# Optimization experiments

Hardware: AMD Instinct MI355X
Metric: run time of the kernel (lower is better)

Reference implementation:

```python
import jax, jax.numpy as jnp
import numpy as np

N = 50000      # nodes
E = 800000     # edges
D_IN = 128
D_H = 512
D_OUT = 256
G = 512        # graphs in batch
EPS_GIN = 0.0  # GINConv default eps
LRELU_SLOPE = 1.5


def setup_inputs() -> dict:
    key = jax.random.key(0)
    ks = jax.random.split(key, 16)
    x = jax.random.normal(ks[0], (N, D_IN), dtype=jnp.float32)
    edge_index = jax.random.randint(ks[1], (2, E), 0, N, dtype=jnp.int64)
    batch = jnp.sort(jax.random.randint(ks[2], (N,), 0, G, dtype=jnp.int64))
    def lin(k, fan_in, fan_out):
        bound = 1.0 / np.sqrt(fan_in)
        k1, k2 = jax.random.split(k)
        W = jax.random.uniform(k1, (fan_in, fan_out), jnp.float32, -bound, bound)
        b = jax.random.uniform(k2, (fan_out,), jnp.float32, -bound, bound)
        return W, b
    W1, b1 = lin(ks[3], D_IN, D_H)
    W2, b2 = lin(ks[4], D_H, D_H)
    W3, b3 = lin(ks[5], D_H, D_H)
    W4, b4 = lin(ks[6], D_H, D_H)
    Wl, bl = lin(ks[7], D_H, D_OUT)
    return {"x": x, "edge_index": edge_index, "batch": batch,
            "W1": W1, "b1": b1, "W2": W2, "b2": b2,
            "W3": W3, "b3": b3, "W4": W4, "b4": b4,
            "Wl": Wl, "bl": bl}


def reference(x, edge_index, batch, W1, b1, W2, b2, W3, b3, W4, b4, Wl, bl):
    # GIN aggregation: sum neighbor (source) features at each target node
    src, dst = edge_index[0], edge_index[1]
    agg = jax.ops.segment_sum(x[src], dst, num_segments=N)  # [N, D_IN]
    h = (1.0 + EPS_GIN) * x + agg
    # 4-layer MLP (Dropout inactive in eval; LeakyReLU negative_slope=1.5)
    h = h @ W1 + b1
    h = jnp.where(h > 0, h, LRELU_SLOPE * h)
    h = jax.nn.relu(h @ W2 + b2)
    h = jax.nn.relu(h @ W3 + b3)
    h = h @ W4 + b4                      # [N, D_H]
    # global mean pool over graphs
    sums = jax.ops.segment_sum(h, batch, num_segments=G)          # [G, D_H]
    cnt = jax.ops.segment_sum(jnp.ones((N, 1), h.dtype), batch, num_segments=G)
    pooled = sums / jnp.maximum(cnt, 1.0)
    out = pooled @ Wl + bl               # [G, D_OUT]
    # F.normalize(dim=1, eps=1e-12)
    nrm = jnp.linalg.norm(out, axis=1, keepdims=True)
    return out / jnp.maximum(nrm, 1e-12)
```

## Files before the change

kernel.cpp:

```cpp
#include <hip/hip_runtime.h>
#include <hip/hip_bf16.h>
#include <cstdint>
#include <cstddef>

#define N_NODES 50000
#define N_EDGES 800000
#define D_IN 128
#define D_H 512
#define D_OUT 256
#define N_GRAPHS 512

#define BM 128
#define BN 256
#define BK 32
#define NBLK ((N_NODES + 255) / 256)
#define CT_SW 264
#define N_MT 391
#define MT_PER_XCD 49

#define NBUCK 196
#define BCAP 6144
#define E_PER_BLK 4096

#define XQ_SCALE 4096.0f
#define XQ_INV (1.0f / 4096.0f)

typedef __bf16 v8bf __attribute__((ext_vector_type(8)));
typedef float v4f __attribute__((ext_vector_type(4)));
typedef int v4i __attribute__((ext_vector_type(4)));

__device__ __forceinline__ float bf2f(unsigned short b) {
  return __uint_as_float(((unsigned int)b) << 16);
}
__device__ __forceinline__ unsigned short f2bf(float f) {
  unsigned int u = __float_as_uint(f);
  u += 0x7FFFu + ((u >> 16) & 1u);
  return (unsigned short)(u >> 16);
}

__device__ __forceinline__ void gload_lds16(const void* g, void* l) {
  __builtin_amdgcn_global_load_lds(
      (const __attribute__((address_space(1))) void*)g,
      (__attribute__((address_space(3))) void*)l, 16, 0, 0);
}

__global__ __launch_bounds__(256) void k_prep(const void* __restrict__ x,
                                              const void* __restrict__ ei,
                                              const void* __restrict__ batch,
                                              int* __restrict__ gcur,
                                              int* __restrict__ flags) {
  __shared__ int cnt[3];
  int t = threadIdx.x;
  gcur[t] = 0;
  if (t < 3) cnt[t] = 0;
  __syncthreads();
  const unsigned short* xs = (const unsigned short*)x;
  int c0 = 0;
  for (int k = t; k < 4096; k += 256) {
    unsigned int e = (xs[k] >> 7) & 0xFFu;
    if (e >= 0x90u) c0++;
  }
  atomicAdd(&cnt[0], c0);
  const int* e32 = (const int*)ei;
  int c1 = 0;
  for (int k = t; k < 512; k += 256)
    if (e32[2 * k + 1] != 0) c1++;
  atomicAdd(&cnt[1], c1);
  const int* b32 = (const int*)batch;
  int c2 = 0;
  {
    int w = (N_NODES - 512) + 2 * t + 1;
    if (b32[w] != 0) c2++;
  }
  atomicAdd(&cnt[2], c2);
  __syncthreads();
  if (t == 0) {
    flags[0] = (cnt[0] > 16) ? 1 : 0;
    flags[1] = (cnt[1] == 0) ? 1 : 0;
    flags[2] = (cnt[2] == 0) ? 1 : 0;
  }
}

__global__ __launch_bounds__(256) void k_transpose_all(
    const void* W1, const void* W2, const void* W3, const void* W4,
    const void* Wl, unsigned short* W1T, unsigned short* W2T,
    unsigned short* W3T, unsigned short* W4T, unsigned short* WlT,
    const int* __restrict__ flags) {
  __shared__ unsigned short tile[64][65];
  int bid = blockIdx.x;
  const void* src;
  unsigned short* dst;
  int R, C, tb;
  if (bid < 16)        { src = W1; dst = W1T; R = 128; C = 512; tb = bid; }
  else if (bid < 80)   { src = W2; dst = W2T; R = 512; C = 512; tb = bid - 16; }
  else if (bid < 144)  { src = W3; dst = W3T; R = 512; C = 512; tb = bid - 80; }
  else if (bid < 208)  { src = W4; dst = W4T; R = 512; C = 512; tb = bid - 144; }
  else                 { src = Wl; dst = WlT; R = 512; C = 256; tb = bid - 208; }
  int tpr = C >> 6;
  int r0 = (tb / tpr) << 6, c0 = (tb % tpr) << 6;
  int t = threadIdx.x;
  bool f32 = flags[0] != 0;
#pragma unroll
  for (int k = 0; k < 16; ++k) {
    int idx = k * 256 + t;
    int r = idx >> 6, c = idx & 63;
    unsigned short v =
        f32 ? f2bf(((const float*)src)[(size_t)(r0 + r) * C + c0 + c])
            : ((const unsigned short*)src)[(size_t)(r0 + r) * C + c0 + c];
    tile[c][r] = v;
  }
  __syncthreads();
#pragma unroll
  for (int k = 0; k < 16; ++k) {
    int idx = k * 256 + t;
    int r = idx >> 6, c = idx & 63;
    dst[(size_t)(c0 + r) * R + r0 + c] = tile[r][c];
  }
}

__global__ __launch_bounds__(256) void k_cvtx(const void* __restrict__ x,
                                              const int* __restrict__ flags,
                                              unsigned int* __restrict__ xi) {
  int i = blockIdx.x * 256 + threadIdx.x;
  if (i >= N_NODES * D_IN / 2) {
    if (i < N_NODES * D_IN / 2 + 64) xi[i] = 0;
    return;
  }
  float v0, v1;
  if (flags[0]) {
    const float* xf = (const float*)x + (size_t)i * 2;
    v0 = xf[0];
    v1 = xf[1];
  } else {
    unsigned int p = ((const unsigned int*)x)[i];
    v0 = __uint_as_float((p & 0xFFFFu) << 16);
    v1 = __uint_as_float(p & 0xFFFF0000u);
  }
  int q0 = __float2int_rn(fminf(fmaxf(v0, -7.99f), 7.99f) * XQ_SCALE);
  int q1 = __float2int_rn(fminf(fmaxf(v1, -7.99f), 7.99f) * XQ_SCALE);
  xi[i] = ((unsigned int)q0 & 0xFFFFu) | ((unsigned int)q1 << 16);
}

__global__ __launch_bounds__(256) void kb_scatter(
    const int* __restrict__ ei, const int* __restrict__ flags,
    int* __restrict__ gcur, unsigned int* __restrict__ pairs, int ne) {
  __shared__ int hist[256];
  __shared__ int sstart[256];
  __shared__ int gbase[256];
  __shared__ int sh[256];
  __shared__ unsigned int lbuf[E_PER_BLK];
  int t = threadIdx.x;
  int e0 = blockIdx.x * E_PER_BLK;
  int nloc = ne - e0;
  if (nloc > E_PER_BLK) nloc = E_PER_BLK;
  hist[t] = 0;
  __syncthreads();
  bool fe64 = flags[1] != 0;
  unsigned int pk[16];
  short bk[16], rk[16];
#pragma unroll
  for (int it = 0; it < 16; ++it) {
    int li = it * 256 + t;
    bk[it] = -1;
    if (li < nloc) {
      size_t e = (size_t)e0 + li;
      int s = fe64 ? ei[2 * e] : ei[e];
      int d = fe64 ? ei[2 * ((size_t)ne + e)] : ei[(size_t)ne + e];
      int b = d >> 8;
      pk[it] = (unsigned int)(s & 0xFFFF) | ((unsigned int)(d & 255) << 16) |
               ((unsigned int)b << 24);
      bk[it] = (short)b;
      rk[it] = (short)atomicAdd(&hist[b], 1);
    }
  }
  __syncthreads();
  int cnt = hist[t];
  sh[t] = cnt;
  __syncthreads();
  for (int o = 1; o < 256; o <<= 1) {
    int a = sh[t];
    int bb = (t >= o) ? sh[t - o] : 0;
    __syncthreads();
    sh[t] = a + bb;
    __syncthreads();
  }
  sstart[t] = sh[t] - cnt;
  gbase[t] = (cnt > 0) ? atomicAdd(&gcur[t], cnt) : 0;
  __syncthreads();
#pragma unroll
  for (int it = 0; it < 16; ++it)
    if (bk[it] >= 0) lbuf[sstart[bk[it]] + rk[it]] = pk[it];
  __syncthreads();
  for (int i = t; i < nloc; i += 256) {
    unsigned int v = lbuf[i];
    int b = v >> 24;
    int off = gbase[b] + (i - sstart[b]);
    if (off < BCAP) pairs[(size_t)b * BCAP + off] = v;
  }
}

__global__ __launch_bounds__(256) void kb_sort(
    const unsigned int* __restrict__ pairs, const int* __restrict__ gcur,
    int* __restrict__ rowptr, unsigned short* __restrict__ elist) {
  __shared__ int sh[256];
  __shared__ int cursor[256];
  __shared__ unsigned int lpair[BCAP];
  __shared__ unsigned short sorted[BCAP];
  int b = blockIdx.x, t = threadIdx.x;
  int c = (t < NBUCK) ? gcur[t] : 0;
  if (c > BCAP) c = BCAP;
  sh[t] = c;
  __syncthreads();
  for (int o = 1; o < 256; o <<= 1) {
    int a = sh[t];
    int v = (t >= o) ? sh[t - o] : 0;
    __syncthreads();
    sh[t] = a + v;
    __syncthreads();
  }
  int base = (b == 0) ? 0 : sh[b - 1];
  int cnt = sh[b] - base;
  cursor[t] = 0;
  __syncthreads();
  for (int i = t; i < cnt; i += 256) {
    unsigned int v = pairs[(size_t)b * BCAP + i];
    lpair[i] = v;
    atomicAdd(&cursor[(v >> 16) & 255], 1);
  }
  __syncthreads();
  int nc = cursor[t];
  sh[t] = nc;
  __syncthreads();
  for (int o = 1; o < 256; o <<= 1) {
    int a = sh[t];
    int v = (t >= o) ? sh[t - o] : 0;
    __syncthreads();
    sh[t] = a + v;
    __syncthreads();
  }
  int nstart = sh[t] - nc;
  cursor[t] = nstart;
  int node = b * 256 + t;
  if (node <= N_NODES) rowptr[node] = base + nstart;
  __syncthreads();
  for (int i = t; i < cnt; i += 256) {
    unsigned int v = lpair[i];
    int r = atomicAdd(&cursor[(v >> 16) & 255], 1);
    sorted[r] = (unsigned short)(v & 0xFFFFu);
  }
  __syncthreads();
  for (int i = t; i < cnt; i += 256)
    elist[base + i] = sorted[i];
}

__global__ __launch_bounds__(256) void k_gather(
    const unsigned int* __restrict__ xi, const int* __restrict__ rowptr,
    const unsigned short* __restrict__ elist, unsigned int* __restrict__ h0) {
  int node = blockIdx.x * 4 + (threadIdx.x >> 6);
  if (node >= N_NODES) return;
  int lane = threadIdx.x & 63;
  int l15 = lane & 15;
  int grp = lane >> 4;
  int s0 = rowptr[node], s1 = rowptr[node + 1];
  int a[8];
  {
    v4i self = (v4i){0, 0, 0, 0};
    if (lane < 16) self = *(const v4i*)(xi + (size_t)node * 64 + l15 * 4);
#pragma unroll
    for (int q = 0; q < 4; ++q) {
      a[2 * q]     = (int)(short)(self[q] & 0xFFFF);
      a[2 * q + 1] = self[q] >> 16;
    }
  }
  for (int j0 = s0; j0 < s1; j0 += 64) {
    int jj = j0 + lane;
    int cnt = s1 - j0;
    cnt = cnt < 64 ? cnt : 64;
    int ev = (jj < s1) ? (int)elist[jj] : N_NODES;
    for (int j = 0; j < cnt; j += 4) {
      int src = __shfl(ev, j + grp, 64);
      v4i p = *(const v4i*)(xi + (size_t)src * 64 + l15 * 4);
#pragma unroll
      for (int q = 0; q < 4; ++q) {
        a[2 * q]     += (int)(short)(p[q] & 0xFFFF);
        a[2 * q + 1] += p[q] >> 16;
      }
    }
  }
#pragma unroll
  for (int k = 0; k < 8; ++k) {
    a[k] += __shfl_xor(a[k], 16, 64);
    a[k] += __shfl_xor(a[k], 32, 64);
  }
  if (lane < 16) {
    v4i o;
#pragma unroll
    for (int q = 0; q < 4; ++q) {
      unsigned int lo = f2bf((float)a[2 * q] * XQ_INV);
      unsigned int hi = f2bf((float)a[2 * q + 1] * XQ_INV);
      o[q] = (int)(lo | (hi << 16));
    }
    *(v4i*)(h0 + (size_t)node * 64 + l15 * 4) = o;
  }
}

template <int ACT, bool OUTF32, bool SWZ>
__global__ __launch_bounds__(512, 4) void gemm_bt(
    const unsigned short* __restrict__ A,
    const unsigned short* __restrict__ BT,
    const void* __restrict__ bias, const int* __restrict__ flags,
    void* __restrict__ Cout, int M, int K, int Nc) {
  __shared__ __align__(16) unsigned short smem[2][BM * BK + BN * BK];

  const int tid  = threadIdx.x;
  const int wave = tid >> 6;
  const int lane = tid & 63;
  const int quad = lane >> 4;
  const int l15  = lane & 15;
  int m0, n0;
  if (SWZ) {
    int xcd = blockIdx.x & 7;
    int l = blockIdx.x >> 3;
    int mt = xcd * MT_PER_XCD + (l >> 1);
    if (mt >= N_MT) return;
    m0 = mt * BM;
    n0 = (l & 1) * BN;
  } else {
    n0 = blockIdx.x * BN;
    m0 = blockIdx.y * BM;
  }
  const int wm = (wave >> 2) * 64;
  const int wn = (wave & 3) * 64;
  const bool fm = flags[0] != 0;

  v4f acc[4][4];
#pragma unroll
  for (int i = 0; i < 4; ++i)
#pragma unroll
    for (int j = 0; j < 4; ++j) acc[i][j] = (v4f){0.f, 0.f, 0.f, 0.f};

  auto stage = [&](int kt, int buf) {
    const int k0 = kt * BK;
    unsigned short* As = smem[buf];
    unsigned short* Bs = smem[buf] + BM * BK;
    {
      int L = tid;
      int row = L >> 2;
      int c = (L & 3) ^ ((row >> 1) & 3);
      int gr = m0 + row;
      gr = gr < M ? gr : (M - 1);
      gload_lds16(A + (size_t)gr * K + (k0 + c * 8), As + (size_t)L * 8);
    }
#pragma unroll
    for (int it = 0; it < 2; ++it) {
      int L = tid + it * 512;
      int row = L >> 2;
      int c = (L & 3) ^ ((row >> 1) & 3);
      int gn = n0 + row;
      gload_lds16(BT + (size_t)gn * K + (k0 + c * 8), Bs + (size_t)L * 8);
    }
  };

  const int nK = K / BK;
  stage(0, 0);
  for (int kt = 0; kt < nK; ++kt) {
    __syncthreads();
    if (kt + 1 < nK) stage(kt + 1, (kt + 1) & 1);
    const unsigned short* As = smem[kt & 1];
    const unsigned short* Bs = smem[kt & 1] + BM * BK;
    v8bf af[4], bfr[4];
#pragma unroll
    for (int mi = 0; mi < 4; ++mi) {
      int r = wm + mi * 16 + l15;
      int s = quad ^ ((r >> 1) & 3);
      af[mi] = *(const v8bf*)(As + (r * 4 + s) * 8);
    }
#pragma unroll
    for (int ni = 0; ni < 4; ++ni) {
      int r = wn + ni * 16 + l15;
      int s = quad ^ ((r >> 1) & 3);
      bfr[ni] = *(const v8bf*)(Bs + (r * 4 + s) * 8);
    }
#pragma unroll
    for (int mi = 0; mi < 4; ++mi)
#pragma unroll
      for (int ni = 0; ni < 4; ++ni)
        acc[mi][ni] = __builtin_amdgcn_mfma_f32_16x16x32_bf16(
            af[mi], bfr[ni], acc[mi][ni], 0, 0, 0);
  }

  float bv[4];
#pragma unroll
  for (int ni = 0; ni < 4; ++ni) {
    int col = n0 + wn + ni * 16 + l15;
    bv[ni] = fm ? ((const float*)bias)[col]
                : bf2f(((const unsigned short*)bias)[col]);
  }
#pragma unroll
  for (int mi = 0; mi < 4; ++mi)
#pragma unroll
    for (int ni = 0; ni < 4; ++ni)
#pragma unroll
      for (int rg = 0; rg < 4; ++rg) {
        float v = acc[mi][ni][rg] + bv[ni];
        if (ACT == 0) v = v > 0.f ? v : 1.5f * v;
        if (ACT == 1) v = v > 0.f ? v : 0.f;
        acc[mi][ni][rg] = v;
      }

  if (OUTF32) {
#pragma unroll
    for (int ni = 0; ni < 4; ++ni) {
      int col = n0 + wn + ni * 16 + l15;
#pragma unroll
      for (int mi = 0; mi < 4; ++mi)
#pragma unroll
        for (int rg = 0; rg < 4; ++rg) {
          int row = m0 + wm + mi * 16 + quad * 4 + rg;
          if (row < M)
            ((float*)Cout)[(size_t)row * Nc + col] = acc[mi][ni][rg];
        }
    }
    return;
  }

  unsigned short* Ct = (unsigned short*)smem;
  __syncthreads();
#pragma unroll
  for (int h = 0; h < 2; ++h) {
    if ((wave >> 2) == h) {
#pragma unroll
      for (int mi = 0; mi < 4; ++mi)
#pragma unroll
        for (int ni = 0; ni < 4; ++ni)
#pragma unroll
          for (int rg = 0; rg < 4; ++rg) {
            int lr = mi * 16 + quad * 4 + rg;
            int c = wn + ni * 16 + l15;
            Ct[lr * CT_SW + c] = f2bf(acc[mi][ni][rg]);
          }
    }
    __syncthreads();
    int rl0 = tid >> 5;
    int ch = tid & 31;
#pragma unroll
    for (int p = 0; p < 4; ++p) {
      int rl = rl0 + p * 16;
      int grow = m0 + h * 64 + rl;
      if (grow < M) {
        v4i val = *(const v4i*)(Ct + rl * CT_SW + ch * 8);
        *(v4i*)((unsigned short*)Cout + (size_t)grow * Nc + n0 + ch * 8) = val;
      }
    }
    __syncthreads();
  }
}

__global__ __launch_bounds__(256) void k_pool(
    const unsigned int* __restrict__ hu, const int* __restrict__ batch,
    const int* __restrict__ flags, unsigned int* __restrict__ pooled) {
  __shared__ int bounds[2];
  __shared__ float red[4][D_H];
  int g = blockIdx.x;
  int t = threadIdx.x;
  int grp = t >> 6, l = t & 63;
  bool b64 = flags[2] != 0;
  if (t < 2) {
    int key = g + t;
    int lo = 0, hi = N_NODES;
    while (lo < hi) {
      int mid = (lo + hi) >> 1;
      int bv = b64 ? batch[2 * (size_t)mid] : batch[mid];
      if (bv < key) lo = mid + 1; else hi = mid;
    }
    bounds[t] = lo;
  }
  __syncthreads();
  int s0 = bounds[0], s1 = bounds[1];
  float a[8];
#pragma unroll
  for (int q = 0; q < 8; ++q) a[q] = 0.f;
  int r = s0 + grp;
  for (; r + 4 < s1; r += 8) {
    v4i p0 = *(const v4i*)(hu + (size_t)r * (D_H / 2) + l * 4);
    v4i p1 = *(const v4i*)(hu + (size_t)(r + 4) * (D_H / 2) + l * 4);
#pragma unroll
    for (int q = 0; q < 4; ++q) {
      a[2 * q]     += __uint_as_float(((unsigned int)p0[q] & 0xFFFFu) << 16);
      a[2 * q + 1] += __uint_as_float((unsigned int)p0[q] & 0xFFFF0000u);
    }
#pragma unroll
    for (int q = 0; q < 4; ++q) {
      a[2 * q]     += __uint_as_float(((unsigned int)p1[q] & 0xFFFFu) << 16);
      a[2 * q + 1] += __uint_as_float((unsigned int)p1[q] & 0xFFFF0000u);
    }
  }
  if (r < s1) {
    v4i p0 = *(const v4i*)(hu + (size_t)r * (D_H / 2) + l * 4);
#pragma unroll
    for (int q = 0; q < 4; ++q) {
      a[2 * q]     += __uint_as_float(((unsigned int)p0[q] & 0xFFFFu) << 16);
      a[2 * q + 1] += __uint_as_float((unsigned int)p0[q] & 0xFFFF0000u);
    }
  }
  *(v4f*)(&red[grp][l * 8])     = (v4f){a[0], a[1], a[2], a[3]};
  *(v4f*)(&red[grp][l * 8 + 4]) = (v4f){a[4], a[5], a[6], a[7]};
  __syncthreads();
  float s0v = ((red[0][2 * t] + red[1][2 * t]) +
               (red[2][2 * t] + red[3][2 * t]));
  float s1v = ((red[0][2 * t + 1] + red[1][2 * t + 1]) +
               (red[2][2 * t + 1] + red[3][2 * t + 1]));
  float inv = 1.0f / fmaxf((float)(s1 - s0), 1.0f);
  unsigned int lo = f2bf(s0v * inv);
  unsigned int hi = f2bf(s1v * inv);
  pooled[(size_t)g * (D_H / 2) + t] = lo | (hi << 16);
}

__global__ __launch_bounds__(256) void k_norm(const float* __restrict__ of,
                                              const int* __restrict__ flags,
                                              void* __restrict__ out) {
  __shared__ float red[4];
  int g = blockIdx.x, t = threadIdx.x;
  float v = of[g * D_OUT + t];
  float s = v * v;
#pragma unroll
  for (int o = 32; o > 0; o >>= 1) s += __shfl_xor(s, o, 64);
  if ((t & 63) == 0) red[t >> 6] = s;
  __syncthreads();
  float tot = red[0] + red[1] + red[2] + red[3];
  float inv = 1.0f / fmaxf(sqrtf(tot), 1e-12f);
  float r = v * inv;
  if (flags[0])
    ((float*)out)[g * D_OUT + t] = r;
  else
    ((unsigned short*)out)[g * D_OUT + t] = f2bf(r);
}

extern "C" void kernel_launch(void* const* d_in, const int* in_sizes, int n_in,
                              void* d_out, int out_size, void* d_ws,
                              size_t ws_size, hipStream_t stream) {
  const void* x    = d_in[0];
  const int* ei    = (const int*)d_in[1];
  const int* batch = (const int*)d_in[2];
  const void* W1 = d_in[3];
  const void* b1 = d_in[4];
  const void* W2 = d_in[5];
  const void* b2 = d_in[6];
  const void* W3 = d_in[7];
  const void* b3 = d_in[8];
  const void* W4 = d_in[9];
  const void* b4 = d_in[10];
  const void* Wl = d_in[11];
  const void* bl = d_in[12];

  char* ws = (char*)d_ws;
  size_t off = 0;
  auto alloc = [&](size_t bytes) {
    void* p = ws + off;
    off += (bytes + 255) & ~(size_t)255;
    return p;
  };
  int* flags           = (int*)alloc(64);
  unsigned short* W1T  = (unsigned short*)alloc((size_t)D_IN * D_H * 2);
  unsigned short* W2T  = (unsigned short*)alloc((size_t)D_H * D_H * 2);
  unsigned short* W3T  = (unsigned short*)alloc((size_t)D_H * D_H * 2);
  unsigned short* W4T  = (unsigned short*)alloc((size_t)D_H * D_H * 2);
  unsigned short* WlT  = (unsigned short*)alloc((size_t)D_H * D_OUT * 2);
  unsigned int* pooled3 = (unsigned int*)alloc((size_t)N_GRAPHS * D_H * 2);
  unsigned int* pooled4 = (unsigned int*)alloc((size_t)N_GRAPHS * D_H * 2);
  float* outf          = (float*)alloc((size_t)N_GRAPHS * D_OUT * 4);
  int* gcur   = (int*)alloc(256 * 4);
  int* rowptr = (int*)alloc(((size_t)N_NODES + 1) * 4);
  unsigned short* elist = (unsigned short*)alloc((size_t)N_EDGES * 2);
  void* S1 = alloc((size_t)N_NODES * D_H * 2);
  void* S2 = alloc((size_t)N_NODES * D_H * 2);
  unsigned int* xi   = (unsigned int*)S1;
  unsigned short* hA = (unsigned short*)S1;
  unsigned int* pairs = (unsigned int*)((char*)S1 + ((size_t)16 << 20));
  unsigned int* h0u  = (unsigned int*)S2;
  unsigned short* h0 = (unsigned short*)S2;
  unsigned short* hB = (unsigned short*)S2;

  k_prep<<<1, 256, 0, stream>>>(x, ei, batch, gcur, flags);

  k_transpose_all<<<240, 256, 0, stream>>>(
      W1, W2, W3, W4, Wl, W1T, W2T, W3T, W4T, WlT, flags);
  k_cvtx<<<(N_NODES * D_IN / 2 + 64 + 255) / 256, 256, 0, stream>>>(x, flags, xi);

  const int gScat = (N_EDGES + E_PER_BLK - 1) / E_PER_BLK;
  kb_scatter<<<gScat, 256, 0, stream>>>(ei, flags, gcur, pairs, N_EDGES);
  kb_sort<<<NBUCK, 256, 0, stream>>>(pairs, gcur, rowptr, elist);
  k_gather<<<(N_NODES + 3) / 4, 256, 0, stream>>>(xi, rowptr, elist, h0u);

  const int gBig = 8 * MT_PER_XCD * 2;
  gemm_bt<0, false, true><<<gBig, 512, 0, stream>>>(h0, W1T, b1, flags, hA, N_NODES, D_IN, D_H);
  gemm_bt<1, false, true><<<gBig, 512, 0, stream>>>(hA, W2T, b2, flags, hB, N_NODES, D_H, D_H);
  gemm_bt<1, false, true><<<gBig, 512, 0, stream>>>(hB, W3T, b3, flags, hA, N_NODES, D_H, D_H);

  k_pool<<<N_GRAPHS, 256, 0, stream>>>((const unsigned int*)hA, batch, flags, pooled3);

  dim3 g4(D_H / BN, N_GRAPHS / BM);
  gemm_bt<2, false, false><<<g4, 512, 0, stream>>>(
      (const unsigned short*)pooled3, W4T, b4, flags, pooled4, N_GRAPHS, D_H, D_H);

  dim3 g5(D_OUT / BN, N_GRAPHS / BM);
  gemm_bt<2, true, false><<<g5, 512, 0, stream>>>(
      (const unsigned short*)pooled4, WlT, bl, flags, outf, N_GRAPHS, D_H, D_OUT);

  k_norm<<<N_GRAPHS, 256, 0, stream>>>(outf, flags, (unsigned short*)d_out);
}
```

Measured before the change: 317.8 us.

## Merge scatter, weight transpose, x conversion into one launch; fuse L2 norm into final GEMM

Combines the edge bucket scatter, weight transpose and x quantization kernels into a single launch that dispatches on block index, sharing one shared-memory buffer. The final linear GEMM now computes per-row sum of squares across waves in shared memory and writes normalized output directly, removing the separate normalize kernel and the fp32 intermediate buffer. This is meant to cut launch overheads and small-kernel tails, at the cost of heterogeneous blocks in one grid.

Result: faster. 297.2 us (-6.5%).

```diff
diff --git a/kernel.cpp b/kernel.cpp
--- a/kernel.cpp
+++ b/kernel.cpp
@@ -21,6 +21,11 @@
 #define NBUCK 196
 #define BCAP 6144
 #define E_PER_BLK 4096
+
+#define SCAT_BLKS 196
+#define TR_BLKS 240
+#define CVTX_BLKS ((N_NODES * D_IN / 2 + 64 + 255) / 256)
+#define MID_BLKS (SCAT_BLKS + TR_BLKS + CVTX_BLKS)
 
 #define XQ_SCALE 4096.0f
 #define XQ_INV (1.0f / 4096.0f)
@@ -81,47 +86,109 @@
   }
 }
 
-__global__ __launch_bounds__(256) void k_transpose_all(
+__global__ __launch_bounds__(256) void k_mid(
+    const void* __restrict__ x, const int* __restrict__ ei,
+    const int* __restrict__ flags,
     const void* W1, const void* W2, const void* W3, const void* W4,
     const void* Wl, unsigned short* W1T, unsigned short* W2T,
     unsigned short* W3T, unsigned short* W4T, unsigned short* WlT,
-    const int* __restrict__ flags) {
-  __shared__ unsigned short tile[64][65];
+    int* __restrict__ gcur, unsigned int* __restrict__ pairs,
+    unsigned int* __restrict__ xi, int ne) {
+  __shared__ __align__(16) char mshm[20480];
   int bid = blockIdx.x;
-  const void* src;
-  unsigned short* dst;
-  int R, C, tb;
-  if (bid < 16)        { src = W1; dst = W1T; R = 128; C = 512; tb = bid; }
-  else if (bid < 80)   { src = W2; dst = W2T; R = 512; C = 512; tb = bid - 16; }
-  else if (bid < 144)  { src = W3; dst = W3T; R = 512; C = 512; tb = bid - 80; }
-  else if (bid < 208)  { src = W4; dst = W4T; R = 512; C = 512; tb = bid - 144; }
-  else                 { src = Wl; dst = WlT; R = 512; C = 256; tb = bid - 208; }
-  int tpr = C >> 6;
-  int r0 = (tb / tpr) << 6, c0 = (tb % tpr) << 6;
   int t = threadIdx.x;
-  bool f32 = flags[0] != 0;
-#pragma unroll
-  for (int k = 0; k < 16; ++k) {
-    int idx = k * 256 + t;
-    int r = idx >> 6, c = idx & 63;
-    unsigned short v =
-        f32 ? f2bf(((const float*)src)[(size_t)(r0 + r) * C + c0 + c])
-            : ((const unsigned short*)src)[(size_t)(r0 + r) * C + c0 + c];
-    tile[c][r] = v;
-  }
-  __syncthreads();
-#pragma unroll
-  for (int k = 0; k < 16; ++k) {
-    int idx = k * 256 + t;
-    int r = idx >> 6, c = idx & 63;
-    dst[(size_t)(c0 + r) * R + r0 + c] = tile[r][c];
-  }
-}
-
-__global__ __launch_bounds__(256) void k_cvtx(const void* __restrict__ x,
-                                              const int* __restrict__ flags,
-                                              unsigned int* __restrict__ xi) {
-  int i = blockIdx.x * 256 + threadIdx.x;
+
+  if (bid < SCAT_BLKS) {
+    int* hist = (int*)mshm;
+    int* sstart = hist + 256;
+    int* gbase = sstart + 256;
+    int* sh = gbase + 256;
+    unsigned int* lbuf = (unsigned int*)(mshm + 4096);
+    int e0 = bid * E_PER_BLK;
+    int nloc = ne - e0;
+    if (nloc > E_PER_BLK) nloc = E_PER_BLK;
+    hist[t] = 0;
+    __syncthreads();
+    bool fe64 = flags[1] != 0;
+    unsigned int pk[16];
+    short bk[16], rk[16];
+#pragma unroll
+    for (int it = 0; it < 16; ++it) {
+      int li = it * 256 + t;
+      bk[it] = -1;
+      if (li < nloc) {
+        size_t e = (size_t)e0 + li;
+        int s = fe64 ? ei[2 * e] : ei[e];
+        int d = fe64 ? ei[2 * ((size_t)ne + e)] : ei[(size_t)ne + e];
+        int b = d >> 8;
+        pk[it] = (unsigned int)(s & 0xFFFF) | ((unsigned int)(d & 255) << 16) |
+                 ((unsigned int)b << 24);
+        bk[it] = (short)b;
+        rk[it] = (short)atomicAdd(&hist[b], 1);
+      }
+    }
+    __syncthreads();
+    int cnt = hist[t];
+    sh[t] = cnt;
+    __syncthreads();
+    for (int o = 1; o < 256; o <<= 1) {
+      int a = sh[t];
+      int bb = (t >= o) ? sh[t - o] : 0;
+      __syncthreads();
+      sh[t] = a + bb;
+      __syncthreads();
+    }
+    sstart[t] = sh[t] - cnt;
+    gbase[t] = (cnt > 0) ? atomicAdd(&gcur[t], cnt) : 0;
+    __syncthreads();
+#pragma unroll
+    for (int it = 0; it < 16; ++it)
+      if (bk[it] >= 0) lbuf[sstart[bk[it]] + rk[it]] = pk[it];
+    __syncthreads();
+    for (int i = t; i < nloc; i += 256) {
+      unsigned int v = lbuf[i];
+      int b = v >> 24;
+      int off = gbase[b] + (i - sstart[b]);
+      if (off < BCAP) pairs[(size_t)b * BCAP + off] = v;
+    }
+    return;
+  }
+
+  if (bid < SCAT_BLKS + TR_BLKS) {
+    typedef unsigned short row65[65];
+    row65* tile = (row65*)mshm;
+    int b2 = bid - SCAT_BLKS;
+    const void* src;
+    unsigned short* dst;
+    int R, C, tb;
+    if (b2 < 16)        { src = W1; dst = W1T; R = 128; C = 512; tb = b2; }
+    else if (b2 < 80)   { src = W2; dst = W2T; R = 512; C = 512; tb = b2 - 16; }
+    else if (b2 < 144)  { src = W3; dst = W3T; R = 512; C = 512; tb = b2 - 80; }
+    else if (b2 < 208)  { src = W4; dst = W4T; R = 512; C = 512; tb = b2 - 144; }
+    else                { src = Wl; dst = WlT; R = 512; C = 256; tb = b2 - 208; }
+    int tpr = C >> 6;
+    int r0 = (tb / tpr) << 6, c0 = (tb % tpr) << 6;
+    bool f32 = flags[0] != 0;
+#pragma unroll
+    for (int k = 0; k < 16; ++k) {
+      int idx = k * 256 + t;
+      int r = idx >> 6, c = idx & 63;
+      unsigned short v =
+          f32 ? f2bf(((const float*)src)[(size_t)(r0 + r) * C + c0 + c])
+              : ((const unsigned short*)src)[(size_t)(r0 + r) * C + c0 + c];
+      tile[c][r] = v;
+    }
+    __syncthreads();
+#pragma unroll
+    for (int k = 0; k < 16; ++k) {
+      int idx = k * 256 + t;
+      int r = idx >> 6, c = idx & 63;
+      dst[(size_t)(c0 + r) * R + r0 + c] = tile[r][c];
+    }
+    return;
+  }
+
+  int i = (bid - SCAT_BLKS - TR_BLKS) * 256 + t;
   if (i >= N_NODES * D_IN / 2) {
     if (i < N_NODES * D_IN / 2 + 64) xi[i] = 0;
     return;
@@ -139,64 +206,6 @@
   int q0 = __float2int_rn(fminf(fmaxf(v0, -7.99f), 7.99f) * XQ_SCALE);
   int q1 = __float2int_rn(fminf(fmaxf(v1, -7.99f), 7.99f) * XQ_SCALE);
   xi[i] = ((unsigned int)q0 & 0xFFFFu) | ((unsigned int)q1 << 16);
-}
-
-__global__ __launch_bounds__(256) void kb_scatter(
-    const int* __restrict__ ei, const int* __restrict__ flags,
-    int* __restrict__ gcur, unsigned int* __restrict__ pairs, int ne) {
-  __shared__ int hist[256];
-  __shared__ int sstart[256];
-  __shared__ int gbase[256];
-  __shared__ int sh[256];
-  __shared__ unsigned int lbuf[E_PER_BLK];
-  int t = threadIdx.x;
-  int e0 = blockIdx.x * E_PER_BLK;
-  int nloc = ne - e0;
-  if (nloc > E_PER_BLK) nloc = E_PER_BLK;
-  hist[t] = 0;
-  __syncthreads();
-  bool fe64 = flags[1] != 0;
-  unsigned int pk[16];
-  short bk[16], rk[16];
-#pragma unroll
-  for (int it = 0; it < 16; ++it) {
-    int li = it * 256 + t;
-    bk[it] = -1;
-    if (li < nloc) {
-      size_t e = (size_t)e0 + li;
-      int s = fe64 ? ei[2 * e] : ei[e];
-      int d = fe64 ? ei[2 * ((size_t)ne + e)] : ei[(size_t)ne + e];
-      int b = d >> 8;
-      pk[it] = (unsigned int)(s & 0xFFFF) | ((unsigned int)(d & 255) << 16) |
-               ((unsigned int)b << 24);
-      bk[it] = (short)b;
-      rk[it] = (short)atomicAdd(&hist[b], 1);
-    }
-  }
-  __syncthreads();
-  int cnt = hist[t];
-  sh[t] = cnt;
-  __syncthreads();
-  for (int o = 1; o < 256; o <<= 1) {
-    int a = sh[t];
-    int bb = (t >= o) ? sh[t - o] : 0;
-    __syncthreads();
-    sh[t] = a + bb;
-    __syncthreads();
-  }
-  sstart[t] = sh[t] - cnt;
-  gbase[t] = (cnt > 0) ? atomicAdd(&gcur[t], cnt) : 0;
-  __syncthreads();
-#pragma unroll
-  for (int it = 0; it < 16; ++it)
-    if (bk[it] >= 0) lbuf[sstart[bk[it]] + rk[it]] = pk[it];
-  __syncthreads();
-  for (int i = t; i < nloc; i += 256) {
-    unsigned int v = lbuf[i];
-    int b = v >> 24;
-    int off = gbase[b] + (i - sstart[b]);
-    if (off < BCAP) pairs[(size_t)b * BCAP + off] = v;
-  }
 }
 
 __global__ __launch_bounds__(256) void kb_sort(
@@ -304,7 +313,7 @@
   }
 }
 
-template <int ACT, bool OUTF32, bool SWZ>
+template <int ACT, int OUT, bool SWZ>
 __global__ __launch_bounds__(512, 4) void gemm_bt(
     const unsigned short* __restrict__ A,
     const unsigned short* __restrict__ BT,
@@ -408,7 +417,7 @@
         acc[mi][ni][rg] = v;
       }
 
-  if (OUTF32) {
+  if (OUT == 1) {
 #pragma unroll
     for (int ni = 0; ni < 4; ++ni) {
       int col = n0 + wn + ni * 16 + l15;
@@ -421,6 +430,53 @@
             ((float*)Cout)[(size_t)row * Nc + col] = acc[mi][ni][rg];
         }
     }
+    return;
+  }
+
+  if (OUT == 2) {
+    float* ssq = (float*)smem;
+    __syncthreads();
+    float pp[4][4];
+#pragma unroll
+    for (int mi = 0; mi < 4; ++mi)
+#pragma unroll
+      for (int rg = 0; rg < 4; ++rg) {
+        float s = 0.f;
+#pragma unroll
+        for (int ni = 0; ni < 4; ++ni) {
+          float v = acc[mi][ni][rg];
+          s += v * v;
+        }
+#pragma unroll
+        for (int o = 1; o < 16; o <<= 1) s += __shfl_xor(s, o, 64);
+        pp[mi][rg] = s;
+      }
+    if (l15 == 0) {
+#pragma unroll
+      for (int mi = 0; mi < 4; ++mi)
+#pragma unroll
+        for (int rg = 0; rg < 4; ++rg)
+          ssq[(wave & 3) * 128 + wm + mi * 16 + quad * 4 + rg] = pp[mi][rg];
+    }
+    __syncthreads();
+#pragma unroll
+    for (int mi = 0; mi < 4; ++mi)
+#pragma unroll
+      for (int rg = 0; rg < 4; ++rg) {
+        int row = wm + mi * 16 + quad * 4 + rg;
+        float tot = (ssq[row] + ssq[128 + row]) + (ssq[256 + row] + ssq[384 + row]);
+        float inv = 1.0f / fmaxf(sqrtf(tot), 1e-12f);
+        int grow = m0 + row;
+#pragma unroll
+        for (int ni = 0; ni < 4; ++ni) {
+          int col = wn + ni * 16 + l15;
+          float r = acc[mi][ni][rg] * inv;
+          if (fm)
+            ((float*)Cout)[(size_t)grow * Nc + col] = r;
+          else
+            ((unsigned short*)Cout)[(size_t)grow * Nc + col] = f2bf(r);
+        }
+      }
     return;
   }
 
@@ -516,26 +572,6 @@
   pooled[(size_t)g * (D_H / 2) + t] = lo | (hi << 16);
 }
 
-__global__ __launch_bounds__(256) void k_norm(const float* __restrict__ of,
-                                              const int* __restrict__ flags,
-                                              void* __restrict__ out) {
-  __shared__ float red[4];
-  int g = blockIdx.x, t = threadIdx.x;
-  float v = of[g * D_OUT + t];
-  float s = v * v;
-#pragma unroll
-  for (int o = 32; o > 0; o >>= 1) s += __shfl_xor(s, o, 64);
-  if ((t & 63) == 0) red[t >> 6] = s;
-  __syncthreads();
-  float tot = red[0] + red[1] + red[2] + red[3];
-  float inv = 1.0f / fmaxf(sqrtf(tot), 1e-12f);
-  float r = v * inv;
-  if (flags[0])
-    ((float*)out)[g * D_OUT + t] = r;
-  else
-    ((unsigned short*)out)[g * D_OUT + t] = f2bf(r);
-}
-
 extern "C" void kernel_launch(void* const* d_in, const int* in_sizes, int n_in,
                               void* d_out, int out_size, void* d_ws,
                               size_t ws_size, hipStream_t stream) {
@@ -568,7 +604,6 @@
   unsigned short* WlT  = (unsigned short*)alloc((size_t)D_H * D_OUT * 2);
   unsigned int* pooled3 = (unsigned int*)alloc((size_t)N_GRAPHS * D_H * 2);
   unsigned int* pooled4 = (unsigned int*)alloc((size_t)N_GRAPHS * D_H * 2);
-  float* outf          = (float*)alloc((size_t)N_GRAPHS * D_OUT * 4);
   int* gcur   = (int*)alloc(256 * 4);
   int* rowptr = (int*)alloc(((size_t)N_NODES + 1) * 4);
   unsigned short* elist = (unsigned short*)alloc((size_t)N_EDGES * 2);
@@ -583,29 +618,25 @@
 
   k_prep<<<1, 256, 0, stream>>>(x, ei, batch, gcur, flags);
 
-  k_transpose_all<<<240, 256, 0, stream>>>(
-      W1, W2, W3, W4, Wl, W1T, W2T, W3T, W4T, WlT, flags);
-  k_cvtx<<<(N_NODES * D_IN / 2 + 64 + 255) / 256, 256, 0, stream>>>(x, flags, xi);
-
-  const int gScat = (N_EDGES + E_PER_BLK - 1) / E_PER_BLK;
-  kb_scatter<<<gScat, 256, 0, stream>>>(ei, flags, gcur, pairs, N_EDGES);
+  k_mid<<<MID_BLKS, 256, 0, stream>>>(
+      x, ei, flags, W1, W2, W3, W4, Wl, W1T, W2T, W3T, W4T, WlT,
+      gcur, pairs, xi, N_EDGES);
+
   kb_sort<<<NBUCK, 256, 0, stream>>>(pairs, gcur, rowptr, elist);
   k_gather<<<(N_NODES + 3) / 4, 256, 0, stream>>>(xi, rowptr, elist, h0u);
 
   const int gBig = 8 * MT_PER_XCD * 2;
-  gemm_bt<0, false, true><<<gBig, 512, 0, stream>>>(h0, W1T, b1, flags, hA, N_NODES, D_IN, D_H);
-  gemm_bt<1, false, true><<<gBig, 512, 0, stream>>>(hA, W2T, b2, flags, hB, N_NODES, D_H, D_H);
-  gemm_bt<1, false, true><<<gBig, 512, 0, stream>>>(hB, W3T, b3, flags, hA, N_NODES, D_H, D_H);
+  gemm_bt<0, 0, true><<<gBig, 512, 0, stream>>>(h0, W1T, b1, flags, hA, N_NODES, D_IN, D_H);
+  gemm_bt<1, 0, true><<<gBig, 512, 0, stream>>>(hA, W2T, b2, flags, hB, N_NODES, D_H, D_H);
+  gemm_bt<1, 0, true><<<gBig, 512, 0, stream>>>(hB, W3T, b3, flags, hA, N_NODES, D_H, D_H);
 
   k_pool<<<N_GRAPHS, 256, 0, stream>>>((const unsigned int*)hA, batch, flags, pooled3);
 
   dim3 g4(D_H / BN, N_GRAPHS / BM);
-  gemm_bt<2, false, false><<<g4, 512, 0, stream>>>(
+  gemm_bt<2, 0, false><<<g4, 512, 0, stream>>>(
       (const unsigned short*)pooled3, W4T, b4, flags, pooled4, N_GRAPHS, D_H, D_H);
 
   dim3 g5(D_OUT / BN, N_GRAPHS / BM);
-  gemm_bt<2, true, false><<<g5, 512, 0, stream>>>(
-      (const unsigned short*)pooled4, WlT, bl, flags, outf, N_GRAPHS, D_H, D_OUT);
-
-  k_norm<<<N_GRAPHS, 256, 0, stream>>>(outf, flags, (unsigned short*)d_out);
-}
+  gemm_bt<2, 2, false><<<g5, 512, 0, stream>>>(
+      (const unsigned short*)pooled4, WlT, bl, flags, d_out, N_GRAPHS, D_H, D_OUT);
+}
```
